# Kernel optimization log

Hardware: AMD Instinct MI355X
Metric: run time of the kernel (lower is better)

Reference implementation:

```python
import jax, jax.numpy as jnp
import numpy as np

B, T, E, D = 8, 2048, 1024, 64  # batch, seq_len, n_emb, head_dim

def setup_inputs() -> dict:
    key = jax.random.key(0)
    ks = jax.random.split(key, 4)
    scale = 1.0 / np.sqrt(E)
    return {
        "x": jax.random.normal(ks[0], (B, T, E), dtype=jnp.float32),
        "Wq": jax.random.normal(ks[1], (E, D), dtype=jnp.float32) * scale,
        "bq": jnp.zeros((D,), dtype=jnp.float32),
        "Wk": jax.random.normal(ks[2], (E, D), dtype=jnp.float32) * scale,
        "bk": jnp.zeros((D,), dtype=jnp.float32),
        "Wv": jax.random.normal(ks[3], (E, D), dtype=jnp.float32) * scale,
        "bv": jnp.zeros((D,), dtype=jnp.float32),
    }

def reference(x, Wq, bq, Wk, bk, Wv, bv):
    # QKV projections: [B,T,E] @ [E,D] -> [B,T,D]
    q = x @ Wq + bq
    k = x @ Wk + bk
    v = x @ Wv + bv
    d = q.shape[-1]
    # scaled dot-product scores [B,T,T]
    wei = jnp.einsum('btd,bsd->bts', q, k) * (d ** -0.5)
    # causal mask: position t attends to s <= t
    t = wei.shape[1]
    causal = jnp.tril(jnp.ones((t, t), dtype=bool))
    wei = jnp.where(causal, wei, -jnp.inf)
    wei = jax.nn.softmax(wei, axis=-1)
    # attention output [B,T,D]
    return jnp.einsum('bts,bsd->btd', wei, v)
```

## Files before the change

### kernel.cpp

```cpp
#include <hip/hip_runtime.h>
#include <math.h>


#define B_   8
#define T_   2048
#define E_   1024
#define D_   64
#define BT_  (B_ * T_)

typedef __attribute__((ext_vector_type(8))) short s16x8;
typedef __attribute__((ext_vector_type(4))) short s16x4;
typedef __attribute__((ext_vector_type(4))) float f32x4;

__device__ __forceinline__ short f2bf(float f) {
    union { float f; unsigned u; } a; a.f = f;
    unsigned r = a.u + 0x7fffu + ((a.u >> 16) & 1u);
    return (short)(r >> 16);
}

#define MFMA16(a, b, c) __builtin_amdgcn_mfma_f32_16x16x32_bf16((a), (b), (c), 0, 0, 0)

typedef __attribute__((address_space(1))) const unsigned int gu32;
typedef __attribute__((address_space(3)))       unsigned int su32;
__device__ __forceinline__ void gld16(const void* g, void* s) {
    __builtin_amdgcn_global_load_lds((gu32*)g, (su32*)s, 16, 0, 0);
}

#define DPPF(x, ctrl) __builtin_bit_cast(float, \
    __builtin_amdgcn_update_dpp(0, __builtin_bit_cast(int, (x)), (ctrl), 0xF, 0xF, true))

__device__ __forceinline__ float rsum16(float x) {
    x += DPPF(x, 0xB1);
    x += DPPF(x, 0x4E);
    x += DPPF(x, 0x124);
    x += DPPF(x, 0x128);
    return x;
}

__global__ __launch_bounds__(256) void wtrans_kernel(
    const float* __restrict__ Wq, const float* __restrict__ Wk,
    const float* __restrict__ Wv, short* __restrict__ Wt)
{
    __shared__ float sT[64][65];
    const int sel = blockIdx.x >> 4;
    const int k0  = (blockIdx.x & 15) * 64;
    const float* W = sel == 0 ? Wq : (sel == 1 ? Wk : Wv);
    const int t  = threadIdx.x;
    const int kr = t >> 4, c4 = (t & 15) * 4;
    #pragma unroll
    for (int i = 0; i < 4; ++i) {
        float4 v = *(const float4*)&W[(size_t)(k0 + kr + i * 16) * D_ + c4];
        sT[kr + i * 16][c4 + 0] = v.x; sT[kr + i * 16][c4 + 1] = v.y;
        sT[kr + i * 16][c4 + 2] = v.z; sT[kr + i * 16][c4 + 3] = v.w;
    }
    __syncthreads();
    #pragma unroll
    for (int i = 0; i < 4; ++i) {
        int n  = (t >> 4) + i * 16;
        int kk = (t & 15) * 4;
        s16x4 o;
        o.x = f2bf(sT[kk + 0][n]); o.y = f2bf(sT[kk + 1][n]);
        o.z = f2bf(sT[kk + 2][n]); o.w = f2bf(sT[kk + 3][n]);
        *(s16x4*)&Wt[(size_t)(sel * 64 + n) * E_ + k0 + kk] = o;
    }
}

__global__ __launch_bounds__(512) void qkv_kernel(
    const float* __restrict__ x, const short* __restrict__ Wt,
    const float* __restrict__ bq, const float* __restrict__ bk,
    const float* __restrict__ bv,
    short* __restrict__ Qg, short* __restrict__ Kg, short* __restrict__ VTg)
{
    __shared__ short sW[2][12 * 16 * 128];
    __shared__ short sX[2][64 * 140];
    const int tid  = threadIdx.x;
    const int lane = tid & 63;
    const int w    = tid >> 6;
    const int l15  = lane & 15, quad = lane >> 4;
    const int h2   = w & 1;
    const int n2   = w >> 1;
    const int t0   = blockIdx.x * 64;
    const int bb   = t0 >> 11;

    const int srow = tid >> 3;
    const int skc  = (tid & 7) * 16;
    const float* px = &x[(size_t)(t0 + srow) * E_ + skc];

    const int lrow = lane >> 4;
    const int lc16 = lane & 15;

    f32x4 acc[3][2];
    #pragma unroll
    for (int a = 0; a < 3; ++a)
        #pragma unroll
        for (int h = 0; h < 2; ++h)
            acc[a][h] = (f32x4){0.f, 0.f, 0.f, 0.f};

    float4 lda0 = *(const float4*)(px +   0);
    float4 lda1 = *(const float4*)(px +   4);
    float4 lda2 = *(const float4*)(px +   8);
    float4 lda3 = *(const float4*)(px +  12);
    float4 ldb0 = *(const float4*)(px + 128);
    float4 ldb1 = *(const float4*)(px + 132);
    float4 ldb2 = *(const float4*)(px + 136);
    float4 ldb3 = *(const float4*)(px + 140);

    #pragma unroll
    for (int j = 0; j < 6; ++j) {
        const int cid = w * 6 + j;
        const int t3g = cid >> 2;
        const int rr  = ((cid & 3) << 2) + lrow;
        const int c16 = lc16 ^ (rr & 7);
        gld16(&Wt[(size_t)(t3g * 16 + rr) * E_ + c16 * 8],
              (char*)&sW[0][0] + cid * 1024);
    }

    int buf = 0;
    for (int k0 = 0; k0 < E_; k0 += 128) {
        s16x8 pk0, pk1;
        pk0[0] = f2bf(lda0.x); pk0[1] = f2bf(lda0.y);
        pk0[2] = f2bf(lda0.z); pk0[3] = f2bf(lda0.w);
        pk0[4] = f2bf(lda1.x); pk0[5] = f2bf(lda1.y);
        pk0[6] = f2bf(lda1.z); pk0[7] = f2bf(lda1.w);
        pk1[0] = f2bf(lda2.x); pk1[1] = f2bf(lda2.y);
        pk1[2] = f2bf(lda2.z); pk1[3] = f2bf(lda2.w);
        pk1[4] = f2bf(lda3.x); pk1[5] = f2bf(lda3.y);
        pk1[6] = f2bf(lda3.z); pk1[7] = f2bf(lda3.w);
        *(s16x8*)&sX[buf][srow * 140 + skc]     = pk0;
        *(s16x8*)&sX[buf][srow * 140 + skc + 8] = pk1;
        __syncthreads();

        lda0 = ldb0; lda1 = ldb1; lda2 = ldb2; lda3 = ldb3;
        if (k0 + 256 < E_) {
            const float* p2 = px + k0 + 256;
            ldb0 = *(const float4*)(p2 +  0);
            ldb1 = *(const float4*)(p2 +  4);
            ldb2 = *(const float4*)(p2 +  8);
            ldb3 = *(const float4*)(p2 + 12);
        }
        if (k0 + 128 < E_) {
            #pragma unroll
            for (int j = 0; j < 6; ++j) {
                const int cid = w * 6 + j;
                const int t3g = cid >> 2;
                const int rr  = ((cid & 3) << 2) + lrow;
                const int c16 = lc16 ^ (rr & 7);
                gld16(&Wt[(size_t)(t3g * 16 + rr) * E_ + k0 + 128 + c16 * 8],
                      (char*)&sW[buf ^ 1][0] + cid * 1024);
            }
        }

        s16x8 aw[3][4];
        #pragma unroll
        for (int t3 = 0; t3 < 3; ++t3) {
            const int tb = (n2 * 3 + t3) * 2048 + l15 * 128;
            #pragma unroll
            for (int kc = 0; kc < 4; ++kc) {
                const int c16 = (kc * 4 + quad) ^ (l15 & 7);
                aw[t3][kc] = *(const s16x8*)&sW[buf][tb + c16 * 8];
            }
        }
        s16x8 bxf[2][4];
        #pragma unroll
        for (int h = 0; h < 2; ++h) {
            const int trow = (h2 * 2 + h) * 16 + l15;
            #pragma unroll
            for (int kc = 0; kc < 4; ++kc)
                bxf[h][kc] = *(const s16x8*)&sX[buf][trow * 140 + kc * 32 + quad * 8];
        }
        #pragma unroll
        for (int t3 = 0; t3 < 3; ++t3)
            #pragma unroll
            for (int h = 0; h < 2; ++h)
                #pragma unroll
                for (int kc = 0; kc < 4; ++kc)
                    acc[t3][h] = MFMA16(aw[t3][kc], bxf[h][kc], acc[t3][h]);
        buf ^= 1;
    }

    __syncthreads();
    short* sVT = &sX[0][0];

    #pragma unroll
    for (int t3 = 0; t3 < 3; ++t3) {
        const int nt = n2 * 3 + t3;
        const int fb = (nt & 3) * 16 + quad * 4;
        const float* bias = nt < 4 ? bq : (nt < 8 ? bk : bv);
        f32x4 bsv = *(const f32x4*)&bias[fb];
        #pragma unroll
        for (int h = 0; h < 2; ++h) {
            const int lt  = (h2 * 2 + h) * 16 + l15;
            const int tok = t0 + lt;
            f32x4 v = acc[t3][h] + bsv;
            if (nt < 4) {
                v *= 0.125f;
                s16x4 o = { f2bf(v[0]), f2bf(v[1]), f2bf(v[2]), f2bf(v[3]) };
                *(s16x4*)&Qg[(size_t)tok * D_ + fb] = o;
            } else if (nt < 8) {
                s16x4 o = { f2bf(v[0]), f2bf(v[1]), f2bf(v[2]), f2bf(v[3]) };
                *(s16x4*)&Kg[(size_t)tok * D_ + fb] = o;
            } else {
                #pragma unroll
                for (int r = 0; r < 4; ++r)
                    sVT[(fb + r) * 72 + lt] = f2bf(v[r]);
            }
        }
    }
    __syncthreads();
    {
        const int d  = tid >> 3;
        const int tq = (tid & 7) * 8;
        s16x8 vv = *(const s16x8*)&sVT[d * 72 + tq];
        *(s16x8*)&VTg[(size_t)(bb * D_ + d) * T_ + (t0 & (T_ - 1)) + tq] = vv;
    }
}

__global__ __launch_bounds__(512) void attn_kernel(
    const short* __restrict__ Qg, const short* __restrict__ Kg,
    const short* __restrict__ VTg, float* __restrict__ out)
{
    __shared__ char smem[141312];
    short* sP = (short*)smem;
    float* sO = (float*)smem;
    float* sl = (float*)(smem + 139264);

    const int tid  = threadIdx.x;
    const int lane = tid & 63;
    const int w    = tid >> 6;
    const int l15  = lane & 15, quad = lane >> 4;
    const int b    = blockIdx.x & 7;
    const int j    = blockIdx.x >> 3;
    const int tq   = j * 64;
    const int nch  = j + 1;
    const int c0   = (w * nch) >> 3;
    const int c1   = ((w + 1) * nch) >> 3;

    s16x8 aq[4][2];
    #pragma unroll
    for (int qt = 0; qt < 4; ++qt) {
        const size_t qoff = ((size_t)b * T_ + tq + qt * 16 + l15) * D_ + quad * 8;
        aq[qt][0] = *(const s16x8*)&Qg[qoff];
        aq[qt][1] = *(const s16x8*)&Qg[qoff + 32];
    }

    f32x4 oo[4][4];
    float lp[4][4];
    #pragma unroll
    for (int qt = 0; qt < 4; ++qt) {
        #pragma unroll
        for (int nt = 0; nt < 4; ++nt)
            oo[qt][nt] = (f32x4){0.f, 0.f, 0.f, 0.f};
        #pragma unroll
        for (int r = 0; r < 4; ++r) lp[qt][r] = 0.f;
    }

    const short* kb = Kg  + (size_t)b * T_ * D_;
    const short* vb = VTg + (size_t)b * D_ * T_;
    short* sPw = sP + w * (4 * 16 * 72);

    for (int cc = c0; cc < c1; ++cc) {
        const int s0 = cc * 64;
        const bool diag = (cc == nch - 1);
        s16x8 bk[4][2];
        #pragma unroll
        for (int nt = 0; nt < 4; ++nt) {
            const short* pk = kb + (size_t)(s0 + nt * 16 + l15) * D_ + quad * 8;
            bk[nt][0] = *(const s16x8*)pk;
            bk[nt][1] = *(const s16x8*)(pk + 32);
        }
        const f32x4 zz = (f32x4){0.f, 0.f, 0.f, 0.f};
        #pragma unroll
        for (int qt = 0; qt < 4; ++qt) {
            f32x4 sacc[4];
            #pragma unroll
            for (int nt = 0; nt < 4; ++nt) {
                sacc[nt] = MFMA16(aq[qt][0], bk[nt][0], zz);
                sacc[nt] = MFMA16(aq[qt][1], bk[nt][1], sacc[nt]);
            }
            float p[4][4];
            #pragma unroll
            for (int nt = 0; nt < 4; ++nt)
                #pragma unroll
                for (int r = 0; r < 4; ++r) {
                    float e = __expf(sacc[nt][r]);
                    if (diag && (s0 + nt * 16 + l15 > tq + qt * 16 + quad * 4 + r))
                        e = 0.f;
                    p[nt][r] = e;
                }
            #pragma unroll
            for (int r = 0; r < 4; ++r)
                lp[qt][r] += (p[0][r] + p[1][r]) + (p[2][r] + p[3][r]);
            #pragma unroll
            for (int nt = 0; nt < 4; ++nt)
                #pragma unroll
                for (int r = 0; r < 4; ++r)
                    sPw[qt * (16 * 72) + (quad * 4 + r) * 72 + nt * 16 + l15] =
                        f2bf(p[nt][r]);
        }
        s16x8 bv[4][2];
        #pragma unroll
        for (int nt = 0; nt < 4; ++nt) {
            const short* pv = vb + (size_t)(nt * 16 + l15) * T_ + s0 + quad * 8;
            bv[nt][0] = *(const s16x8*)pv;
            bv[nt][1] = *(const s16x8*)(pv + 32);
        }
        #pragma unroll
        for (int qt = 0; qt < 4; ++qt) {
            s16x8 ap0 = *(const s16x8*)&sPw[qt * (16 * 72) + l15 * 72 + quad * 8];
            s16x8 ap1 = *(const s16x8*)&sPw[qt * (16 * 72) + l15 * 72 + 32 + quad * 8];
            #pragma unroll
            for (int nt = 0; nt < 4; ++nt) {
                oo[qt][nt] = MFMA16(ap0, bv[nt][0], oo[qt][nt]);
                oo[qt][nt] = MFMA16(ap1, bv[nt][1], oo[qt][nt]);
            }
        }
    }

    f32x4 lv[4];
    #pragma unroll
    for (int qt = 0; qt < 4; ++qt)
        #pragma unroll
        for (int r = 0; r < 4; ++r)
            lv[qt][r] = rsum16(lp[qt][r]);

    __syncthreads();
    {
        float* sOw = sO + w * (64 * 68);
        #pragma unroll
        for (int qt = 0; qt < 4; ++qt)
            #pragma unroll
            for (int nt = 0; nt < 4; ++nt)
                *(f32x4*)&sOw[(nt * 16 + l15) * 68 + qt * 16 + quad * 4] = oo[qt][nt];
        if (l15 == 0) {
            #pragma unroll
            for (int qt = 0; qt < 4; ++qt)
                *(f32x4*)&sl[w * 64 + qt * 16 + quad * 4] = lv[qt];
        }
    }
    __syncthreads();
    {
        const int d  = tid & 63;
        const int rb = (tid >> 6) * 8;
        f32x4 osum0 = (f32x4){0.f, 0.f, 0.f, 0.f};
        f32x4 osum1 = (f32x4){0.f, 0.f, 0.f, 0.f};
        f32x4 lsum0 = (f32x4){0.f, 0.f, 0.f, 0.f};
        f32x4 lsum1 = (f32x4){0.f, 0.f, 0.f, 0.f};
        #pragma unroll
        for (int w2 = 0; w2 < 8; ++w2) {
            const float* so  = &sO[w2 * (64 * 68) + d * 68 + rb];
            const float* slp = &sl[w2 * 64 + rb];
            osum0 += *(const f32x4*)(so);
            osum1 += *(const f32x4*)(so + 4);
            lsum0 += *(const f32x4*)(slp);
            lsum1 += *(const f32x4*)(slp + 4);
        }
        #pragma unroll
        for (int i = 0; i < 4; ++i)
            out[((size_t)b * T_ + tq + rb + i) * D_ + d] = osum0[i] / lsum0[i];
        #pragma unroll
        for (int i = 0; i < 4; ++i)
            out[((size_t)b * T_ + tq + rb + 4 + i) * D_ + d] = osum1[i] / lsum1[i];
    }
}

extern "C" void kernel_launch(void* const* d_in, const int* in_sizes, int n_in,
                              void* d_out, int out_size, void* d_ws, size_t ws_size,
                              hipStream_t stream) {
    (void)in_sizes; (void)n_in; (void)out_size; (void)ws_size;
    const float* x  = (const float*)d_in[0];
    const float* Wq = (const float*)d_in[1];
    const float* bq = (const float*)d_in[2];
    const float* Wk = (const float*)d_in[3];
    const float* bk = (const float*)d_in[4];
    const float* Wv = (const float*)d_in[5];
    const float* bv = (const float*)d_in[6];

    char* ws = (char*)d_ws;
    short* Qg  = (short*)(ws);
    short* Kg  = (short*)(ws + (size_t)2 * 1024 * 1024);
    short* VTg = (short*)(ws + (size_t)4 * 1024 * 1024);
    short* Wt  = (short*)(ws + (size_t)6 * 1024 * 1024);

    wtrans_kernel<<<48, 256, 0, stream>>>(Wq, Wk, Wv, Wt);
    qkv_kernel<<<BT_ / 64, 512, 0, stream>>>(x, Wt, bq, bk, bv, Qg, Kg, VTg);
    attn_kernel<<<B_ * 32, 512, 0, stream>>>(Qg, Kg, VTg, (float*)d_out);
}
```

Baseline: 135.3 us.

## Split long causal query tiles across two blocks and merge partials

```diff
diff --git a/kernel.cpp b/kernel.cpp
--- a/kernel.cpp
+++ b/kernel.cpp
@@ -217,7 +217,8 @@
 
 __global__ __launch_bounds__(512) void attn_kernel(
     const short* __restrict__ Qg, const short* __restrict__ Kg,
-    const short* __restrict__ VTg, float* __restrict__ out)
+    const short* __restrict__ VTg, float* __restrict__ pws,
+    float* __restrict__ out)
 {
     __shared__ char smem[141312];
     short* sP = (short*)smem;
@@ -229,11 +230,28 @@
     const int w    = tid >> 6;
     const int l15  = lane & 15, quad = lane >> 4;
     const int b    = blockIdx.x & 7;
-    const int j    = blockIdx.x >> 3;
-    const int tq   = j * 64;
-    const int nch  = j + 1;
-    const int c0   = (w * nch) >> 3;
-    const int c1   = ((w + 1) * nch) >> 3;
+    const int s    = blockIdx.x >> 3;
+
+    int j, g0, g1, kk = 0;
+    bool split;
+    if (s < 32) {
+        split = true;
+        j  = 31 - (s >> 1);
+        kk = s & 1;
+        const int nc = j + 1, h = nc >> 1;
+        g0 = kk ? h : 0;
+        g1 = kk ? nc : h;
+    } else {
+        split = false;
+        j  = 47 - s;
+        g0 = 0;
+        g1 = j + 1;
+    }
+    const int nch = j + 1;
+    const int tq  = j * 64;
+    const int nwk = g1 - g0;
+    const int c0  = g0 + ((w * nwk) >> 3);
+    const int c1  = g0 + (((w + 1) * nwk) >> 3);
 
     s16x8 aq[4][2];
     #pragma unroll
@@ -354,12 +372,48 @@
             lsum0 += *(const f32x4*)(slp);
             lsum1 += *(const f32x4*)(slp + 4);
         }
-        #pragma unroll
-        for (int i = 0; i < 4; ++i)
-            out[((size_t)b * T_ + tq + rb + i) * D_ + d] = osum0[i] / lsum0[i];
-        #pragma unroll
-        for (int i = 0; i < 4; ++i)
-            out[((size_t)b * T_ + tq + rb + 4 + i) * D_ + d] = osum1[i] / lsum1[i];
+        if (!split) {
+            #pragma unroll
+            for (int i = 0; i < 4; ++i)
+                out[((size_t)b * T_ + tq + rb + i) * D_ + d] = osum0[i] / lsum0[i];
+            #pragma unroll
+            for (int i = 0; i < 4; ++i)
+                out[((size_t)b * T_ + tq + rb + 4 + i) * D_ + d] = osum1[i] / lsum1[i];
+        } else {
+            const int idx = (((b << 4) | (j - 16)) << 1) | kk;
+            float* pO = pws + (size_t)idx * 4160;
+            #pragma unroll
+            for (int i = 0; i < 4; ++i)
+                pO[(rb + i) * 64 + d] = osum0[i];
+            #pragma unroll
+            for (int i = 0; i < 4; ++i)
+                pO[(rb + 4 + i) * 64 + d] = osum1[i];
+            if (d == 0) {
+                #pragma unroll
+                for (int i = 0; i < 4; ++i) pO[4096 + rb + i]     = lsum0[i];
+                #pragma unroll
+                for (int i = 0; i < 4; ++i) pO[4096 + rb + 4 + i] = lsum1[i];
+            }
+        }
+    }
+}
+
+__global__ __launch_bounds__(256) void amerge_kernel(
+    const float* __restrict__ pws, float* __restrict__ out)
+{
+    const int b  = blockIdx.x & 7;
+    const int jj = blockIdx.x >> 3;
+    const int tq = (jj + 16) * 64;
+    const float* O0 = pws + (size_t)((((b << 4) | jj) << 1) + 0) * 4160;
+    const float* O1 = pws + (size_t)((((b << 4) | jj) << 1) + 1) * 4160;
+    const int d  = threadIdx.x & 63;
+    const int r0 = (threadIdx.x >> 6) * 16;
+    #pragma unroll
+    for (int i = 0; i < 16; ++i) {
+        const int r = r0 + i;
+        const float o = O0[r * 64 + d] + O1[r * 64 + d];
+        const float l = O0[4096 + r]   + O1[4096 + r];
+        out[((size_t)b * T_ + tq + r) * D_ + d] = o / l;
     }
 }
 
@@ -380,8 +434,10 @@
     short* Kg  = (short*)(ws + (size_t)2 * 1024 * 1024);
     short* VTg = (short*)(ws + (size_t)4 * 1024 * 1024);
     short* Wt  = (short*)(ws + (size_t)6 * 1024 * 1024);
+    float* pws = (float*)(ws + (size_t)8 * 1024 * 1024);
 
     wtrans_kernel<<<48, 256, 0, stream>>>(Wq, Wk, Wv, Wt);
     qkv_kernel<<<BT_ / 64, 512, 0, stream>>>(x, Wt, bq, bk, bv, Qg, Kg, VTg);
-    attn_kernel<<<B_ * 32, 512, 0, stream>>>(Qg, Kg, VTg, (float*)d_out);
-}
+    attn_kernel<<<B_ * 48, 512, 0, stream>>>(Qg, Kg, VTg, pws, (float*)d_out);
+    amerge_kernel<<<128, 256, 0, stream>>>(pws, (float*)d_out);
+}
```

Result: slower. 143.1 us (+5.7%).
